# Kernel tuning notes

Measured on AMD Instinct MI355X. Metric: run time of the kernel, lower is better.

The kernel has to match this reference:

```python
import jax, jax.numpy as jnp
import numpy as np
import math

B, L, H, NH = 4, 2048, 2048, 16
HD = H // NH  # head_dim = 128
ROPE_BASE = 10000.0


def rotate_half(x):
    x1, x2 = jnp.split(x, 2, axis=-1)
    return jnp.concatenate((-x2, x1), axis=-1)


def rope_cos_sin(seq_len, dim, dtype=jnp.float32):
    inv_freq = 1.0 / (ROPE_BASE ** (jnp.arange(0, dim, 2, dtype=jnp.float32) / dim))
    t = jnp.arange(seq_len, dtype=jnp.float32)
    freqs = jnp.outer(t, inv_freq)              # [L, dim/2]
    emb = jnp.concatenate((freqs, freqs), -1)   # [L, dim]
    return jnp.cos(emb).astype(dtype), jnp.sin(emb).astype(dtype)


def setup_inputs() -> dict:
    key = jax.random.key(0)
    ks = jax.random.split(key, 5)
    x = jax.random.normal(ks[0], (B, L, H), dtype=jnp.float32)
    # causal mask, broadcastable over [B, NH, L, L]; 0 -> masked
    mask = jnp.tril(jnp.ones((L, L), dtype=jnp.int32))[None, None]
    s = 0.02
    Wq = jax.random.normal(ks[1], (H, H), dtype=jnp.float32) * s
    Wk = jax.random.normal(ks[2], (H, H), dtype=jnp.float32) * s
    Wv = jax.random.normal(ks[3], (H, H), dtype=jnp.float32) * s
    Wo = jax.random.normal(ks[4], (H, H), dtype=jnp.float32) * s
    return {"x": x, "mask": mask, "Wq": Wq, "Wk": Wk, "Wv": Wv, "Wo": Wo}


def reference(x, mask, Wq, Wk, Wv, Wo):
    b, l, _ = x.shape
    # nn.Linear: y = x @ W.T (weight shape [out, in])
    q = (x @ Wq.T).reshape(b, l, NH, HD).transpose(0, 2, 1, 3)  # [B,H,L,D]
    k = (x @ Wk.T).reshape(b, l, NH, HD).transpose(0, 2, 1, 3)
    v = (x @ Wv.T).reshape(b, l, NH, HD).transpose(0, 2, 1, 3)
    cos, sin = rope_cos_sin(l, HD, x.dtype)  # [L, D] broadcasts over [B,H,L,D]
    q = q * cos + rotate_half(q) * sin
    k = k * cos + rotate_half(k) * sin
    attn = jnp.einsum("bhqd,bhkd->bhqk", q, k) / math.sqrt(HD)
    attn = jnp.where(mask == 0, jnp.float32(-jnp.inf), attn)
    attn = jax.nn.softmax(attn.astype(jnp.float32), axis=-1).astype(x.dtype)
    out = jnp.einsum("bhqk,bhkd->bhqd", attn, v)
    out = out.transpose(0, 2, 1, 3).reshape(b, l, NH * HD)
    return out @ Wo.T
```

## Files before the change

### kernel.cpp

```cpp
#include <hip/hip_runtime.h>
#include <cstdint>
#include <cmath>

#define B_   4
#define L_   2048
#define H_   2048
#define NH_  16
#define HD_  128
#define ML_  (B_*L_)

using short8 = __attribute__((ext_vector_type(8))) short;
using f32x4  = __attribute__((ext_vector_type(4))) float;
using f32x16 = __attribute__((ext_vector_type(16))) float;
using uint4v = __attribute__((ext_vector_type(4))) unsigned;

__device__ inline short f2bf(float f){
  unsigned u = __builtin_bit_cast(unsigned, f);
  unsigned r = u + 0x7FFFu + ((u >> 16) & 1u);
  return (short)(r >> 16);
}
__device__ inline float bf2f(short s){
  unsigned u = ((unsigned)(unsigned short)s) << 16;
  return __builtin_bit_cast(float, u);
}

#define GLD16(gp, lp) __builtin_amdgcn_global_load_lds(                      \
    (const __attribute__((address_space(1))) void*)(gp),                     \
    (__attribute__((address_space(3))) void*)(lp), 16, 0, 0)

__device__ inline unsigned cvtpk_bf16(float lo, float hi){
  unsigned d;
  asm("v_cvt_pk_bf16_f32 %0, %1, %2" : "=v"(d) : "v"(lo), "v"(hi));
  return d;
}
__device__ inline void permswap32(unsigned &a, unsigned &b){
  asm volatile("v_permlane32_swap_b32 %0, %1" : "+v"(a), "+v"(b));
}
__device__ inline float cross_half_max(float x){
  return fmaxf(x, __shfl_xor(x, 32));
}
__device__ inline float cross_half_add(float x){
  return x + __shfl_xor(x, 32);
}

__device__ inline void cvt8(const float* __restrict__ in, short* __restrict__ out,
                            int i){
  const float4* p = (const float4*)(in + (size_t)i * 8);
  float4 a = p[0], b = p[1];
  short8 s;
  s[0]=f2bf(a.x); s[1]=f2bf(a.y); s[2]=f2bf(a.z); s[3]=f2bf(a.w);
  s[4]=f2bf(b.x); s[5]=f2bf(b.y); s[6]=f2bf(b.z); s[7]=f2bf(b.w);
  *(short8*)(out + (size_t)i * 8) = s;
}

__global__ void rope_table(float* __restrict__ cosT, float* __restrict__ sinT){
  int idx = blockIdx.x * 256 + threadIdx.x;
  if (idx >= L_ * 64) return;
  int l = idx >> 6, d = idx & 63;
  float invf = powf(10000.0f, -(float)d * (1.0f/64.0f));
  float fr = (float)l * invf;
  cosT[idx] = cosf(fr);
  sinT[idx] = sinf(fr);
}

__global__ __launch_bounds__(256)
void cvt_bf16(const float* __restrict__ in, short* __restrict__ out, int n8){
  int i = blockIdx.x * 256 + threadIdx.x;
  if (i >= n8) return;
  cvt8(in, out, i);
}

__global__ __launch_bounds__(256)
void prep(const float* __restrict__ x,  const float* __restrict__ Wq,
          const float* __restrict__ Wk, const float* __restrict__ Wv,
          const float* __restrict__ Wo, short* __restrict__ xb,
          short* __restrict__ Wb, short* __restrict__ WoB,
          float* __restrict__ cosT, float* __restrict__ sinT)
{
  const int blk = blockIdx.x, tid = threadIdx.x;
  const int per = H_ * H_ / 8;
  if (blk < 8192) {
    cvt8(x, xb, blk * 256 + tid);
  } else if (blk < 14336) {
    int i = (blk - 8192) * 256 + tid;
    const float* src; int j;
    if (i < per)          { src = Wq; j = i; }
    else if (i < 2 * per) { src = Wk; j = i - per; }
    else                  { src = Wv; j = i - 2 * per; }
    const float4* p = (const float4*)(src + (size_t)j * 8);
    float4 a = p[0], b = p[1];
    short8 s;
    s[0]=f2bf(a.x); s[1]=f2bf(a.y); s[2]=f2bf(a.z); s[3]=f2bf(a.w);
    s[4]=f2bf(b.x); s[5]=f2bf(b.y); s[6]=f2bf(b.z); s[7]=f2bf(b.w);
    *(short8*)(Wb + (size_t)i * 8) = s;
  } else if (blk < 16384) {
    cvt8(Wo, WoB, (blk - 14336) * 256 + tid);
  } else {
    int idx = (blk - 16384) * 256 + tid;
    int l = idx >> 6, d = idx & 63;
    float invf = powf(10000.0f, -(float)d * (1.0f/64.0f));
    float fr = (float)l * invf;
    cosT[idx] = cosf(fr);
    sinT[idx] = sinf(fr);
  }
}

template<int QKV, int OUT_F32>
__global__ __launch_bounds__(512, 2)
void gemm256_bt(const short* __restrict__ A, const short* __restrict__ Bw,
                void* __restrict__ C0, void* __restrict__ C1,
                void* __restrict__ C2)
{
  constexpr int K = 2048, N = 2048;
  __shared__ short sA[4][256 * 32];
  __shared__ short sB[4][256 * 32];
  const int tid  = threadIdx.x;
  const int lane = tid & 63;
  const int wave = tid >> 6;
  const int wr = wave >> 2, wc = wave & 3;
  const int ln = lane & 15, g = lane >> 4;

  const int blk = blockIdx.x;
  int n_t, m_t;
  if constexpr (QKV) { int i = blk >> 3; n_t = (blk & 7) + 8 * (i >> 5); m_t = i & 31; }
  else               { n_t = blk & 7;    m_t = blk >> 3; }
  const int m0 = m_t * 256;
  const int nb0 = n_t * 256;

  const int u0 = wave * 64 + lane;
  const int u1 = u0 + 512;
  const int r0 = u0 >> 2, c0 = (((u0 & 3) ^ (r0 & 3) ^ ((r0 >> 2) & 3))) * 8;
  const int r1 = u1 >> 2, c1 = (((u1 & 3) ^ (r1 & 3) ^ ((r1 >> 2) & 3))) * 8;

  f32x4 acc[8][4];
  #pragma unroll
  for (int m = 0; m < 8; m++)
    #pragma unroll
    for (int n = 0; n < 4; n++) acc[m][n] = {0.f, 0.f, 0.f, 0.f};

#define STAGE256(T) do {                                                     \
    const int _b = (T) & 3; const int _k = (T) * 32;                         \
    GLD16(A  + (size_t)(m0 + r0) * K + _k + c0, &sA[_b][wave * 512]);        \
    GLD16(A  + (size_t)(m0 + r1) * K + _k + c1, &sA[_b][4096 + wave * 512]); \
    GLD16(Bw + (size_t)(nb0 + r0) * K + _k + c0, &sB[_b][wave * 512]);       \
    GLD16(Bw + (size_t)(nb0 + r1) * K + _k + c1, &sB[_b][4096 + wave * 512]);\
  } while (0)

#define TILE256(T, VMN, PF) do {                                             \
    asm volatile("s_waitcnt vmcnt(" #VMN ")" ::: "memory");                  \
    __builtin_amdgcn_s_barrier();                                            \
    asm volatile("" ::: "memory");                                           \
    const short* _at = &sA[(T) & 3][0];                                      \
    const short* _bt = &sB[(T) & 3][0];                                      \
    short8 af[8], bfr[4];                                                    \
    const int _sl = (g ^ (ln & 3) ^ ((ln >> 2) & 3)) * 8;                    \
    _Pragma("unroll")                                                        \
    for (int m = 0; m < 8; m++)                                              \
      af[m] = *(const short8*)(_at + (wr * 128 + m * 16 + ln) * 32 + _sl);   \
    _Pragma("unroll")                                                        \
    for (int n = 0; n < 4; n++)                                              \
      bfr[n] = *(const short8*)(_bt + (wc * 64 + n * 16 + ln) * 32 + _sl);   \
    if (PF) STAGE256((T) + 3);                                               \
    __builtin_amdgcn_s_setprio(1);                                           \
    _Pragma("unroll")                                                        \
    for (int m = 0; m < 8; m++)                                              \
      _Pragma("unroll")                                                      \
      for (int n = 0; n < 4; n++)                                            \
        acc[m][n] = __builtin_amdgcn_mfma_f32_16x16x32_bf16(af[m], bfr[n],   \
                                                            acc[m][n], 0, 0, 0); \
    __builtin_amdgcn_s_setprio(0);                                           \
  } while (0)

  STAGE256(0); STAGE256(1); STAGE256(2);

  for (int t = 0; t < 61; ++t) TILE256(t, 8, true);
  TILE256(61, 8, false);
  TILE256(62, 4, false);
  TILE256(63, 0, false);

#undef STAGE256
#undef TILE256

  void* Cp; int cb;
  if constexpr (QKV) {
    int w = n_t >> 3;
    Cp = (w == 0) ? C0 : (w == 1) ? C1 : C2;
    cb = (n_t & 7) * 256;
  } else { Cp = C0; cb = nb0; }
  #pragma unroll
  for (int m = 0; m < 8; m++)
    #pragma unroll
    for (int n = 0; n < 4; n++)
      #pragma unroll
      for (int r = 0; r < 4; r++) {
        int row = m0 + wr * 128 + m * 16 + g * 4 + r;
        int col = cb + wc * 64 + n * 16 + ln;
        float v = acc[m][n][r];
        if constexpr (OUT_F32) ((float*)Cp)[(size_t)row * N + col] = v;
        else                   ((short*)Cp)[(size_t)row * N + col] = f2bf(v);
      }
}

__global__ __launch_bounds__(256)
void post_qkv(const short* __restrict__ Vb, short* __restrict__ VT,
              short* __restrict__ Kb,
              const float* __restrict__ cosT, const float* __restrict__ sinT)
{
  __shared__ short t[64 * 64];
  const int tid = threadIdx.x;
  if (blockIdx.x < 4096) {
    const int blk = blockIdx.x;
    const int dt = blk & 1, lt = (blk >> 1) & 31, bh = blk >> 6;
    const int b = bh >> 4, h = bh & 15;
    const int l0 = lt * 64, d0 = dt * 64;
    #pragma unroll
    for (int i = 0; i < 2; i++) {
      int u = tid + i * 256;
      int r = u >> 3, c = u & 7;
      short8 v = *(const short8*)(Vb + ((size_t)b * L_ + l0 + r) * H_ + h * HD_ + d0 + c * 8);
      *(short8*)&t[r * 64 + ((c ^ ((r >> 3) & 7)) << 3)] = v;
    }
    __syncthreads();
    #pragma unroll
    for (int i = 0; i < 2; i++) {
      int u = tid + i * 256;
      int d = u >> 3, lc = u & 7;
      short8 o;
      #pragma unroll
      for (int j = 0; j < 8; j++) {
        int l = lc * 8 + j;
        o[j] = t[l * 64 + (((d >> 3) ^ (lc & 7)) << 3) + (d & 7)];
      }
      *(short8*)(VT + ((size_t)bh * HD_ + d0 + d) * L_ + l0 + lc * 8) = o;
    }
  } else {
    int idx = (blockIdx.x - 4096) * 256 + tid;
    int row = idx >> 7;
    int rem = idx & 127;
    int h = rem >> 3, ch = rem & 7;
    int l = row & (L_ - 1);
    short* base = Kb + (size_t)row * H_ + h * HD_ + ch * 8;
    short8 lo = *(short8*)base;
    short8 hi = *(short8*)(base + 64);
    const float* cp = cosT + l * 64 + ch * 8;
    const float* sp = sinT + l * 64 + ch * 8;
    short8 nlo, nhi;
    #pragma unroll
    for (int j = 0; j < 8; j++) {
      float c = cp[j], s = sp[j];
      float x0 = bf2f(lo[j]), x1 = bf2f(hi[j]);
      nlo[j] = f2bf(x0 * c - x1 * s);
      nhi[j] = f2bf(x1 * c + x0 * s);
    }
    *(short8*)base        = nlo;
    *(short8*)(base + 64) = nhi;
  }
}

__global__ __launch_bounds__(512, 2)
void flash_attn(const short* __restrict__ Qb, const short* __restrict__ Kb,
                const short* __restrict__ VT, short* __restrict__ AO,
                const float* __restrict__ cosT, const float* __restrict__ sinT)
{
  __shared__ short lds_k[2][64 * 128];
  __shared__ short lds_v[2][128 * 64];
  __shared__ float f_lds[8][32];

  const int blk = blockIdx.x;
  int bh, j;
  if (blk < 256) { bh = blk & 63; j = 7 - (blk >> 6); }
  else           { int u = blk - 256; bh = u & 63; j = 3 - (u >> 6); }
  const int q0 = j * 256;
  const int T  = 4 * j + 4;
  const int h = bh & 15, b = bh >> 4;
  const int tid = threadIdx.x, wave = tid >> 6, lane = tid & 63;
  const int hi = lane >> 5, l31 = lane & 31;
  const size_t rowbase = (size_t)b * L_;
  const int colbase = h * HD_;
  const short* Kbh  = Kb + rowbase * H_ + colbase;
  const short* VTbh = VT + (size_t)bh * HD_ * L_;
  const int qw = q0 + wave * 32;
  const int qabs = qw + l31;
  const int fsw = (l31 & 7) ^ ((l31 >> 3) & 3);

  short8 qf[8];
  {
    const short* qp = Qb + (rowbase + qabs) * H_ + colbase + hi * 8;
    short8 qraw[8];
    #pragma unroll
    for (int c = 0; c < 8; c++) qraw[c] = *(const short8*)(qp + c * 16);
    const int lq = qabs & (L_ - 1);
    const float* cp = cosT + lq * 64 + hi * 8;
    const float* sp = sinT + lq * 64 + hi * 8;
    #pragma unroll
    for (int c = 0; c < 4; c++) {
      #pragma unroll
      for (int jj = 0; jj < 8; jj++) {
        float cc = cp[c * 16 + jj], ss = sp[c * 16 + jj];
        float lo = bf2f(qraw[c][jj]), hv = bf2f(qraw[c + 4][jj]);
        qf[c][jj]     = f2bf((lo * cc - hv * ss) * 0.08838834764831845f);
        qf[c + 4][jj] = f2bf((hv * cc + lo * ss) * 0.08838834764831845f);
      }
    }
  }

  f32x16 acc_o[4];
  #pragma unroll
  for (int d = 0; d < 4; d++)
    #pragma unroll
    for (int r = 0; r < 16; r++) acc_o[d][r] = 0.f;
  float m_ = -__builtin_inff(), l_ = 0.f;

  auto stage = [&](int k0s, int bufi) {
    #pragma unroll
    for (int i = 0; i < 2; i++) {
      int c = wave * 2 + i;
      {
        int rt = c * 4 + (lane >> 4);
        int cg = (lane & 15) ^ (rt & 7) ^ ((rt >> 3) & 3);
        const short* gp = Kbh + (size_t)(k0s + rt) * H_ + cg * 8;
        GLD16(gp, &lds_k[bufi][c * 512]);
      }
      {
        int rd = c * 8 + (lane >> 3);
        int cg = (lane & 7) ^ (rd & 7) ^ ((rd >> 3) & 3);
        const short* gp = VTbh + (size_t)rd * L_ + k0s + cg * 8;
        GLD16(gp, &lds_v[bufi][c * 512]);
      }
    }
  };

  stage(0, 0);
  __syncthreads();

  for (int t = 0; t < T; ++t) {
    const int k0 = t * 64;
    if (t + 1 < T) stage((t + 1) * 64, (t + 1) & 1);
    const short* kb_ = lds_k[t & 1];
    const short* vb_ = lds_v[t & 1];

    if (k0 <= qw + 31) {
      f32x16 p0, p1;
      #pragma unroll
      for (int r = 0; r < 16; r++) { p0[r] = 0.f; p1[r] = 0.f; }
      __builtin_amdgcn_s_setprio(1);
      #pragma unroll
      for (int c = 0; c < 8; c++) {
        int ch = (c * 2 + hi) ^ fsw;
        short8 kf0 = *(const short8*)(kb_ + l31 * 128 + ch * 8);
        short8 kf1 = *(const short8*)(kb_ + (32 + l31) * 128 + ch * 8);
        p0 = __builtin_amdgcn_mfma_f32_32x32x16_bf16(kf0, qf[c], p0, 0, 0, 0);
        p1 = __builtin_amdgcn_mfma_f32_32x32x16_bf16(kf1, qf[c], p1, 0, 0, 0);
      }
      __builtin_amdgcn_s_setprio(0);

      if (k0 + 63 > qw) {
        #pragma unroll
        for (int r = 0; r < 16; r++) {
          int kvl = (r & 3) + 8 * (r >> 2) + 4 * hi;
          if (k0 + kvl > qabs)      p0[r] = -__builtin_inff();
          if (k0 + 32 + kvl > qabs) p1[r] = -__builtin_inff();
        }
      }

      float mt = p0[0];
      #pragma unroll
      for (int r = 1; r < 16; r++) mt = fmaxf(mt, p0[r]);
      #pragma unroll
      for (int r = 0; r < 16; r++) mt = fmaxf(mt, p1[r]);
      mt = cross_half_max(mt);
      if (!__all(mt <= m_ + 8.0f)) {
        float mnew = fmaxf(m_, mt);
        float f = __expf(m_ - mnew);
        m_ = mnew;
        l_ *= f;
        if (lane < 32) f_lds[wave][lane] = f;
        f32x4 fr[4];
        #pragma unroll
        for (int i = 0; i < 4; i++)
          fr[i] = *(const f32x4*)&f_lds[wave][i * 8 + hi * 4];
        #pragma unroll
        for (int d = 0; d < 4; d++)
          #pragma unroll
          for (int r = 0; r < 16; r++) acc_o[d][r] *= fr[r >> 2][r & 3];
      }
      float ls = 0.f;
      #pragma unroll
      for (int r = 0; r < 16; r++) { p0[r] = __expf(p0[r] - m_); ls += p0[r]; }
      #pragma unroll
      for (int r = 0; r < 16; r++) { p1[r] = __expf(p1[r] - m_); ls += p1[r]; }
      ls = cross_half_add(ls);
      l_ += ls;

      __builtin_amdgcn_s_setprio(1);
      #pragma unroll
      for (int ks = 0; ks < 4; ks++) {
        const f32x16 &pp = (ks < 2) ? p0 : p1;
        const int kk = (ks & 1) * 8;
        unsigned a0 = cvtpk_bf16(pp[kk + 0], pp[kk + 1]);
        unsigned b0 = cvtpk_bf16(pp[kk + 4], pp[kk + 5]);
        permswap32(a0, b0);
        unsigned a1 = cvtpk_bf16(pp[kk + 2], pp[kk + 3]);
        unsigned b1 = cvtpk_bf16(pp[kk + 6], pp[kk + 7]);
        permswap32(a1, b1);
        uint4v w; w[0] = a0; w[1] = a1; w[2] = b0; w[3] = b1;
        short8 af = __builtin_bit_cast(short8, w);
        #pragma unroll
        for (int db = 0; db < 4; db++) {
          int d  = db * 32 + l31;
          int ch = (ks * 2 + hi) ^ fsw;
          short8 vf = *(const short8*)(vb_ + d * 64 + ch * 8);
          acc_o[db] = __builtin_amdgcn_mfma_f32_32x32x16_bf16(af, vf, acc_o[db], 0, 0, 0);
        }
      }
      __builtin_amdgcn_s_setprio(0);
    }
    __syncthreads();
  }

  if (lane < 32) f_lds[wave][lane] = 1.0f / l_;
  f32x4 lr[4];
  #pragma unroll
  for (int i = 0; i < 4; i++)
    lr[i] = *(const f32x4*)&f_lds[wave][i * 8 + hi * 4];
  #pragma unroll
  for (int db = 0; db < 4; db++)
    #pragma unroll
    for (int r = 0; r < 16; r++) {
      int row = qw + (r & 3) + 8 * (r >> 2) + 4 * hi;
      AO[(rowbase + row) * H_ + colbase + db * 32 + l31] =
          f2bf(acc_o[db][r] * lr[r >> 2][r & 3]);
    }
}

extern "C" void kernel_launch(void* const* d_in, const int* in_sizes, int n_in,
                              void* d_out, int out_size, void* d_ws, size_t ws_size,
                              hipStream_t stream)
{
  const float* x  = (const float*)d_in[0];
  const float* Wq = (const float*)d_in[2];
  const float* Wk = (const float*)d_in[3];
  const float* Wv = (const float*)d_in[4];
  const float* Wo = (const float*)d_in[5];
  float* out = (float*)d_out;

  char* ws = (char*)d_ws;
  const size_t SZ = (size_t)ML_ * H_ * sizeof(short);
  short* Qb = (short*)(ws);
  short* Kb = (short*)(ws + SZ);
  short* Vb = (short*)(ws + 2 * SZ);
  short* xb = (short*)(ws + 3 * SZ);
  short* VT = xb;
  short* AO = Vb;
  float* cosT = (float*)(ws + 4 * SZ);
  float* sinT = cosT + (size_t)L_ * 64;
  short* Wb  = (short*)(ws + 4 * SZ + (size_t)(1 << 20));
  short* WoB = Wb + (size_t)3 * H_ * H_;
  const size_t NEED_FUSED = 4 * SZ + (1 << 20) + (size_t)4 * H_ * H_ * sizeof(short);
  const bool fused = ws_size >= NEED_FUSED;

  if (fused) {
    prep<<<16896, 256, 0, stream>>>(x, Wq, Wk, Wv, Wo, xb, Wb, WoB, cosT, sinT);
    gemm256_bt<1, 0><<<768, 512, 0, stream>>>(xb, Wb, Qb, Kb, Vb);
    post_qkv<<<8192, 256, 0, stream>>>(Vb, VT, Kb, cosT, sinT);
    flash_attn<<<512, 512, 0, stream>>>(Qb, Kb, VT, AO, cosT, sinT);
    gemm256_bt<0, 1><<<256, 512, 0, stream>>>(AO, WoB, out, out, out);
  } else {
    rope_table<<<512, 256, 0, stream>>>(cosT, sinT);
    cvt_bf16<<<ML_ * H_ / 8 / 256, 256, 0, stream>>>(x, xb, ML_ * H_ / 8);
    cvt_bf16<<<H_ * H_ / 8 / 256, 256, 0, stream>>>(Wq, Wb, H_ * H_ / 8);
    gemm256_bt<0, 0><<<256, 512, 0, stream>>>(xb, Wb, Qb, Qb, Qb);
    cvt_bf16<<<H_ * H_ / 8 / 256, 256, 0, stream>>>(Wk, Wb, H_ * H_ / 8);
    gemm256_bt<0, 0><<<256, 512, 0, stream>>>(xb, Wb, Kb, Kb, Kb);
    cvt_bf16<<<H_ * H_ / 8 / 256, 256, 0, stream>>>(Wv, Wb, H_ * H_ / 8);
    gemm256_bt<0, 0><<<256, 512, 0, stream>>>(xb, Wb, Vb, Vb, Vb);
    post_qkv<<<8192, 256, 0, stream>>>(Vb, VT, Kb, cosT, sinT);
    flash_attn<<<512, 512, 0, stream>>>(Qb, Kb, VT, AO, cosT, sinT);
    cvt_bf16<<<H_ * H_ / 8 / 256, 256, 0, stream>>>(Wo, Wb, H_ * H_ / 8);
    gemm256_bt<0, 1><<<256, 512, 0, stream>>>(AO, Wb, out, out, out);
  }
}
```

Measured before the change: 437.1 us.

## Give each flash-attention wave two 32-row query tiles sharing K/V fragments

Halves the block to 4 waves and has each wave compute two 32-row query sub-tiles (64 rows), so every K and V fragment read from LDS feeds two MFMAs instead of one. This cuts LDS read traffic per FLOP. The cost is twice the accumulator and Q registers, which forces launch_bounds down to 1 block of 256 threads per CU and lowers occupancy. It also reorders the second half of the block schedule so the lighter query tiles run in ascending order.

```diff
diff --git a/kernel.cpp b/kernel.cpp
--- a/kernel.cpp
+++ b/kernel.cpp
@@ -257,19 +257,19 @@
   }
 }
 
-__global__ __launch_bounds__(512, 2)
+__global__ __launch_bounds__(256, 1)
 void flash_attn(const short* __restrict__ Qb, const short* __restrict__ Kb,
                 const short* __restrict__ VT, short* __restrict__ AO,
                 const float* __restrict__ cosT, const float* __restrict__ sinT)
 {
   __shared__ short lds_k[2][64 * 128];
   __shared__ short lds_v[2][128 * 64];
-  __shared__ float f_lds[8][32];
+  __shared__ float f_lds[4][64];
 
   const int blk = blockIdx.x;
   int bh, j;
   if (blk < 256) { bh = blk & 63; j = 7 - (blk >> 6); }
-  else           { int u = blk - 256; bh = u & 63; j = 3 - (u >> 6); }
+  else           { int u = blk - 256; bh = u & 63; j = u >> 6; }
   const int q0 = j * 256;
   const int T  = 4 * j + 4;
   const int h = bh & 15, b = bh >> 4;
@@ -279,12 +279,12 @@
   const int colbase = h * HD_;
   const short* Kbh  = Kb + rowbase * H_ + colbase;
   const short* VTbh = VT + (size_t)bh * HD_ * L_;
-  const int qw = q0 + wave * 32;
-  const int qabs = qw + l31;
+  const int qw = q0 + wave * 64;
+  const int qA = qw + l31, qB = qw + 32 + l31;
   const int fsw = (l31 & 7) ^ ((l31 >> 3) & 3);
 
-  short8 qf[8];
-  {
+  short8 qfA[8], qfB[8];
+  auto load_q = [&](int qabs, short8* qf) {
     const short* qp = Qb + (rowbase + qabs) * H_ + colbase + hi * 8;
     short8 qraw[8];
     #pragma unroll
@@ -302,19 +302,22 @@
         qf[c + 4][jj] = f2bf((hv * cc + lo * ss) * 0.08838834764831845f);
       }
     }
-  }
-
-  f32x16 acc_o[4];
+  };
+  load_q(qA, qfA);
+  load_q(qB, qfB);
+
+  f32x16 acc_o[8];
   #pragma unroll
-  for (int d = 0; d < 4; d++)
+  for (int d = 0; d < 8; d++)
     #pragma unroll
     for (int r = 0; r < 16; r++) acc_o[d][r] = 0.f;
-  float m_ = -__builtin_inff(), l_ = 0.f;
+  float mA = -__builtin_inff(), lA = 0.f;
+  float mB = -__builtin_inff(), lB = 0.f;
 
   auto stage = [&](int k0s, int bufi) {
     #pragma unroll
-    for (int i = 0; i < 2; i++) {
-      int c = wave * 2 + i;
+    for (int i = 0; i < 4; i++) {
+      int c = wave * 4 + i;
       {
         int rt = c * 4 + (lane >> 4);
         int cg = (lane & 15) ^ (rt & 7) ^ ((rt >> 3) & 3);
@@ -339,18 +342,20 @@
     const short* kb_ = lds_k[t & 1];
     const short* vb_ = lds_v[t & 1];
 
-    if (k0 <= qw + 31) {
-      f32x16 p0, p1;
+    if (k0 <= qw + 63) {
+      f32x16 pA0, pA1, pB0, pB1;
       #pragma unroll
-      for (int r = 0; r < 16; r++) { p0[r] = 0.f; p1[r] = 0.f; }
+      for (int r = 0; r < 16; r++) { pA0[r]=0.f; pA1[r]=0.f; pB0[r]=0.f; pB1[r]=0.f; }
       __builtin_amdgcn_s_setprio(1);
       #pragma unroll
       for (int c = 0; c < 8; c++) {
         int ch = (c * 2 + hi) ^ fsw;
         short8 kf0 = *(const short8*)(kb_ + l31 * 128 + ch * 8);
         short8 kf1 = *(const short8*)(kb_ + (32 + l31) * 128 + ch * 8);
-        p0 = __builtin_amdgcn_mfma_f32_32x32x16_bf16(kf0, qf[c], p0, 0, 0, 0);
-        p1 = __builtin_amdgcn_mfma_f32_32x32x16_bf16(kf1, qf[c], p1, 0, 0, 0);
+        pA0 = __builtin_amdgcn_mfma_f32_32x32x16_bf16(kf0, qfA[c], pA0, 0, 0, 0);
+        pB0 = __builtin_amdgcn_mfma_f32_32x32x16_bf16(kf0, qfB[c], pB0, 0, 0, 0);
+        pA1 = __builtin_amdgcn_mfma_f32_32x32x16_bf16(kf1, qfA[c], pA1, 0, 0, 0);
+        pB1 = __builtin_amdgcn_mfma_f32_32x32x16_bf16(kf1, qfB[c], pB1, 0, 0, 0);
       }
       __builtin_amdgcn_s_setprio(0);
 
@@ -358,59 +363,101 @@
         #pragma unroll
         for (int r = 0; r < 16; r++) {
           int kvl = (r & 3) + 8 * (r >> 2) + 4 * hi;
-          if (k0 + kvl > qabs)      p0[r] = -__builtin_inff();
-          if (k0 + 32 + kvl > qabs) p1[r] = -__builtin_inff();
+          if (k0 + kvl > qA)      pA0[r] = -__builtin_inff();
+          if (k0 + 32 + kvl > qA) pA1[r] = -__builtin_inff();
+          if (k0 + kvl > qB)      pB0[r] = -__builtin_inff();
+          if (k0 + 32 + kvl > qB) pB1[r] = -__builtin_inff();
         }
       }
 
-      float mt = p0[0];
-      #pragma unroll
-      for (int r = 1; r < 16; r++) mt = fmaxf(mt, p0[r]);
-      #pragma unroll
-      for (int r = 0; r < 16; r++) mt = fmaxf(mt, p1[r]);
-      mt = cross_half_max(mt);
-      if (!__all(mt <= m_ + 8.0f)) {
-        float mnew = fmaxf(m_, mt);
-        float f = __expf(m_ - mnew);
-        m_ = mnew;
-        l_ *= f;
-        if (lane < 32) f_lds[wave][lane] = f;
-        f32x4 fr[4];
-        #pragma unroll
-        for (int i = 0; i < 4; i++)
-          fr[i] = *(const f32x4*)&f_lds[wave][i * 8 + hi * 4];
-        #pragma unroll
-        for (int d = 0; d < 4; d++)
+      {
+        float mt = pA0[0];
+        #pragma unroll
+        for (int r = 1; r < 16; r++) mt = fmaxf(mt, pA0[r]);
+        #pragma unroll
+        for (int r = 0; r < 16; r++) mt = fmaxf(mt, pA1[r]);
+        mt = cross_half_max(mt);
+        if (!__all(mt <= mA + 8.0f)) {
+          float mnew = fmaxf(mA, mt);
+          float f = __expf(mA - mnew);
+          mA = mnew;
+          lA *= f;
+          if (lane < 32) f_lds[wave][lane] = f;
+          f32x4 fr[4];
           #pragma unroll
-          for (int r = 0; r < 16; r++) acc_o[d][r] *= fr[r >> 2][r & 3];
-      }
-      float ls = 0.f;
-      #pragma unroll
-      for (int r = 0; r < 16; r++) { p0[r] = __expf(p0[r] - m_); ls += p0[r]; }
-      #pragma unroll
-      for (int r = 0; r < 16; r++) { p1[r] = __expf(p1[r] - m_); ls += p1[r]; }
-      ls = cross_half_add(ls);
-      l_ += ls;
+          for (int i = 0; i < 4; i++)
+            fr[i] = *(const f32x4*)&f_lds[wave][i * 8 + hi * 4];
+          #pragma unroll
+          for (int d = 0; d < 4; d++)
+            #pragma unroll
+            for (int r = 0; r < 16; r++) acc_o[d][r] *= fr[r >> 2][r & 3];
+        }
+        float ls = 0.f;
+        #pragma unroll
+        for (int r = 0; r < 16; r++) { pA0[r] = __expf(pA0[r] - mA); ls += pA0[r]; }
+        #pragma unroll
+        for (int r = 0; r < 16; r++) { pA1[r] = __expf(pA1[r] - mA); ls += pA1[r]; }
+        lA += cross_half_add(ls);
+      }
+      {
+        float mt = pB0[0];
+        #pragma unroll
+        for (int r = 1; r < 16; r++) mt = fmaxf(mt, pB0[r]);
+        #pragma unroll
+        for (int r = 0; r < 16; r++) mt = fmaxf(mt, pB1[r]);
+        mt = cross_half_max(mt);
+        if (!__all(mt <= mB + 8.0f)) {
+          float mnew = fmaxf(mB, mt);
+          float f = __expf(mB - mnew);
+          mB = mnew;
+          lB *= f;
+          if (lane < 32) f_lds[wave][32 + lane] = f;
+          f32x4 fr[4];
+          #pragma unroll
+          for (int i = 0; i < 4; i++)
+            fr[i] = *(const f32x4*)&f_lds[wave][32 + i * 8 + hi * 4];
+          #pragma unroll
+          for (int d = 0; d < 4; d++)
+            #pragma unroll
+            for (int r = 0; r < 16; r++) acc_o[4 + d][r] *= fr[r >> 2][r & 3];
+        }
+        float ls = 0.f;
+        #pragma unroll
+        for (int r = 0; r < 16; r++) { pB0[r] = __expf(pB0[r] - mB); ls += pB0[r]; }
+        #pragma unroll
+        for (int r = 0; r < 16; r++) { pB1[r] = __expf(pB1[r] - mB); ls += pB1[r]; }
+        lB += cross_half_add(ls);
+      }
 
       __builtin_amdgcn_s_setprio(1);
       #pragma unroll
       for (int ks = 0; ks < 4; ks++) {
-        const f32x16 &pp = (ks < 2) ? p0 : p1;
+        const f32x16 &ppA = (ks < 2) ? pA0 : pA1;
+        const f32x16 &ppB = (ks < 2) ? pB0 : pB1;
         const int kk = (ks & 1) * 8;
-        unsigned a0 = cvtpk_bf16(pp[kk + 0], pp[kk + 1]);
-        unsigned b0 = cvtpk_bf16(pp[kk + 4], pp[kk + 5]);
+        unsigned a0 = cvtpk_bf16(ppA[kk + 0], ppA[kk + 1]);
+        unsigned b0 = cvtpk_bf16(ppA[kk + 4], ppA[kk + 5]);
         permswap32(a0, b0);
-        unsigned a1 = cvtpk_bf16(pp[kk + 2], pp[kk + 3]);
-        unsigned b1 = cvtpk_bf16(pp[kk + 6], pp[kk + 7]);
+        unsigned a1 = cvtpk_bf16(ppA[kk + 2], ppA[kk + 3]);
+        unsigned b1 = cvtpk_bf16(ppA[kk + 6], ppA[kk + 7]);
         permswap32(a1, b1);
-        uint4v w; w[0] = a0; w[1] = a1; w[2] = b0; w[3] = b1;
-        short8 af = __builtin_bit_cast(short8, w);
+        uint4v wA; wA[0] = a0; wA[1] = a1; wA[2] = b0; wA[3] = b1;
+        short8 afA = __builtin_bit_cast(short8, wA);
+        unsigned c0 = cvtpk_bf16(ppB[kk + 0], ppB[kk + 1]);
+        unsigned d0 = cvtpk_bf16(ppB[kk + 4], ppB[kk + 5]);
+        permswap32(c0, d0);
+        unsigned c1 = cvtpk_bf16(ppB[kk + 2], ppB[kk + 3]);
+        unsigned d1 = cvtpk_bf16(ppB[kk + 6], ppB[kk + 7]);
+        permswap32(c1, d1);
+        uint4v wB; wB[0] = c0; wB[1] = c1; wB[2] = d0; wB[3] = d1;
+        short8 afB = __builtin_bit_cast(short8, wB);
         #pragma unroll
         for (int db = 0; db < 4; db++) {
           int d  = db * 32 + l31;
           int ch = (ks * 2 + hi) ^ fsw;
           short8 vf = *(const short8*)(vb_ + d * 64 + ch * 8);
-          acc_o[db] = __builtin_amdgcn_mfma_f32_32x32x16_bf16(af, vf, acc_o[db], 0, 0, 0);
+          acc_o[db]     = __builtin_amdgcn_mfma_f32_32x32x16_bf16(afA, vf, acc_o[db], 0, 0, 0);
+          acc_o[4 + db] = __builtin_amdgcn_mfma_f32_32x32x16_bf16(afB, vf, acc_o[4 + db], 0, 0, 0);
         }
       }
       __builtin_amdgcn_s_setprio(0);
@@ -418,18 +465,25 @@
     __syncthreads();
   }
 
-  if (lane < 32) f_lds[wave][lane] = 1.0f / l_;
-  f32x4 lr[4];
+  if (lane < 32) {
+    f_lds[wave][lane]      = 1.0f / lA;
+    f_lds[wave][32 + lane] = 1.0f / lB;
+  }
+  f32x4 lrA[4], lrB[4];
   #pragma unroll
-  for (int i = 0; i < 4; i++)
-    lr[i] = *(const f32x4*)&f_lds[wave][i * 8 + hi * 4];
+  for (int i = 0; i < 4; i++) {
+    lrA[i] = *(const f32x4*)&f_lds[wave][i * 8 + hi * 4];
+    lrB[i] = *(const f32x4*)&f_lds[wave][32 + i * 8 + hi * 4];
+  }
   #pragma unroll
   for (int db = 0; db < 4; db++)
     #pragma unroll
     for (int r = 0; r < 16; r++) {
-      int row = qw + (r & 3) + 8 * (r >> 2) + 4 * hi;
-      AO[(rowbase + row) * H_ + colbase + db * 32 + l31] =
-          f2bf(acc_o[db][r] * lr[r >> 2][r & 3]);
+      int crow = (r & 3) + 8 * (r >> 2) + 4 * hi;
+      AO[(rowbase + qw + crow) * H_ + colbase + db * 32 + l31] =
+          f2bf(acc_o[db][r] * lrA[r >> 2][r & 3]);
+      AO[(rowbase + qw + 32 + crow) * H_ + colbase + db * 32 + l31] =
+          f2bf(acc_o[4 + db][r] * lrB[r >> 2][r & 3]);
     }
 }
 
@@ -463,7 +517,7 @@
     prep<<<16896, 256, 0, stream>>>(x, Wq, Wk, Wv, Wo, xb, Wb, WoB, cosT, sinT);
     gemm256_bt<1, 0><<<768, 512, 0, stream>>>(xb, Wb, Qb, Kb, Vb);
     post_qkv<<<8192, 256, 0, stream>>>(Vb, VT, Kb, cosT, sinT);
-    flash_attn<<<512, 512, 0, stream>>>(Qb, Kb, VT, AO, cosT, sinT);
+    flash_attn<<<512, 256, 0, stream>>>(Qb, Kb, VT, AO, cosT, sinT);
     gemm256_bt<0, 1><<<256, 512, 0, stream>>>(AO, WoB, out, out, out);
   } else {
     rope_table<<<512, 256, 0, stream>>>(cosT, sinT);
@@ -475,7 +529,7 @@
     cvt_bf16<<<H_ * H_ / 8 / 256, 256, 0, stream>>>(Wv, Wb, H_ * H_ / 8);
     gemm256_bt<0, 0><<<256, 512, 0, stream>>>(xb, Wb, Vb, Vb, Vb);
     post_qkv<<<8192, 256, 0, stream>>>(Vb, VT, Kb, cosT, sinT);
-    flash_attn<<<512, 512, 0, stream>>>(Qb, Kb, VT, AO, cosT, sinT);
+    flash_attn<<<512, 256, 0, stream>>>(Qb, Kb, VT, AO, cosT, sinT);
     cvt_bf16<<<H_ * H_ / 8 / 256, 256, 0, stream>>>(Wo, Wb, H_ * H_ / 8);
     gemm256_bt<0, 1><<<256, 512, 0, stream>>>(AO, Wb, out, out, out);
   }
```

After: 498.1 us. +13.9%, slower.
